# Performance work log

Measured on AMD Instinct MI355X. Metric: run time of the kernel, lower is better.

Reference implementation:

```python
import jax, jax.numpy as jnp
import numpy as np

B, T, C, H = 4, 2048, 1024, 16
D = C // H  # head dim = 64


def setup_inputs() -> dict:
    key = jax.random.key(0)
    k_x, k_wa, k_ba, k_wp, k_bp = jax.random.split(key, 5)
    s = 1.0 / np.sqrt(C)
    return {
        "x": jax.random.normal(k_x, (B, T, C), dtype=jnp.float32),
        "w_attn": jax.random.uniform(k_wa, (C, 3 * C), minval=-s, maxval=s, dtype=jnp.float32),
        "b_attn": jax.random.uniform(k_ba, (3 * C,), minval=-s, maxval=s, dtype=jnp.float32),
        "w_proj": jax.random.uniform(k_wp, (C, C), minval=-s, maxval=s, dtype=jnp.float32),
        "b_proj": jax.random.uniform(k_bp, (C,), minval=-s, maxval=s, dtype=jnp.float32),
    }


def reference(x, w_attn, b_attn, w_proj, b_proj):
    b, t, c = x.shape
    qkv = x @ w_attn + b_attn  # [b, t, 3c]
    q, k, v = jnp.split(qkv, 3, axis=-1)
    # [b, h, t, d]
    q = q.reshape(b, t, H, D).transpose(0, 2, 1, 3)
    k = k.reshape(b, t, H, D).transpose(0, 2, 1, 3)
    v = v.reshape(b, t, H, D).transpose(0, 2, 1, 3)
    scale = 1.0 / np.sqrt(D)
    logits = jnp.einsum("bhqd,bhkd->bhqk", q, k) * scale
    causal = jnp.tril(jnp.ones((t, t), dtype=bool))
    logits = jnp.where(causal, logits, jnp.finfo(logits.dtype).min)
    attn = jax.nn.softmax(logits, axis=-1)
    y = jnp.einsum("bhqk,bhkd->bhqd", attn, v)
    y = y.transpose(0, 2, 1, 3).reshape(b, t, c)
    return y @ w_proj + b_proj
```

## Files before the change

kernel.cpp:

```cpp
#include <hip/hip_runtime.h>


using u16 = unsigned short;
using u32 = unsigned int;
using bf16x8 = __attribute__((ext_vector_type(8))) __bf16;
using f32x4  = __attribute__((ext_vector_type(4))) float;
using f32x16 = __attribute__((ext_vector_type(16))) float;
using u16x8  = __attribute__((ext_vector_type(8))) u16;
using u16x4  = __attribute__((ext_vector_type(4))) u16;
using u32x2  = __attribute__((ext_vector_type(2))) u32;
using u32x4  = __attribute__((ext_vector_type(4))) u32;
using fvec4  = __attribute__((ext_vector_type(4))) float;

__device__ __forceinline__ u16 f2bf(float f) {
  u32 u = __builtin_bit_cast(u32, f);
  u32 r = (u + 0x7FFFu + ((u >> 16) & 1u)) >> 16;
  return (u16)r;
}

__device__ __forceinline__ u32 cvtpk(float lo, float hi) {
  u32 r;
  asm("v_cvt_pk_bf16_f32 %0, %1, %2" : "=v"(r) : "v"(lo), "v"(hi));
  return r;
}

__device__ __forceinline__ f32x4 mfma16(bf16x8 a, bf16x8 b, f32x4 c) {
  return __builtin_amdgcn_mfma_f32_16x16x32_bf16(a, b, c, 0, 0, 0);
}

__device__ __forceinline__ f32x16 mfma32(bf16x8 a, bf16x8 b, f32x16 c) {
  return __builtin_amdgcn_mfma_f32_32x32x16_bf16(a, b, c, 0, 0, 0);
}

__device__ __forceinline__ void gld16(const u16* g, u16* l) {
  __builtin_amdgcn_global_load_lds(
      (const __attribute__((address_space(1))) void*)g,
      (__attribute__((address_space(3))) void*)l, 16, 0, 0);
}

__device__ __forceinline__ void lgkm_barrier() {
  asm volatile("s_waitcnt lgkmcnt(0)" ::: "memory");
  __builtin_amdgcn_s_barrier();
  __builtin_amdgcn_sched_barrier(0);
}

__global__ __launch_bounds__(256) void conv_kernel(
    const float* __restrict__ in, u16* __restrict__ out) {
  const size_t i = ((size_t)blockIdx.x * 256 + threadIdx.x) * 8;
  fvec4 a = *(const fvec4*)(in + i);
  fvec4 b = *(const fvec4*)(in + i + 4);
  u16x8 h;
#pragma unroll
  for (int j = 0; j < 4; ++j) { h[j] = f2bf(a[j]); h[4 + j] = f2bf(b[j]); }
  *(u16x8*)(out + i) = h;
}

__global__ __launch_bounds__(256) void transpose_conv_kernel(
    const float* __restrict__ W, u16* __restrict__ Wt, int K, int N) {
  __shared__ float tile[32][33];
  const int n0 = blockIdx.x * 32, k0 = blockIdx.y * 32;
  const int tx = threadIdx.x, ty = threadIdx.y;
#pragma unroll
  for (int j = 0; j < 4; ++j)
    tile[ty + j * 8][tx] = W[(size_t)(k0 + ty + j * 8) * N + n0 + tx];
  __syncthreads();
#pragma unroll
  for (int j = 0; j < 4; ++j)
    Wt[(size_t)(n0 + ty + j * 8) * K + k0 + tx] = f2bf(tile[tx][ty + j * 8]);
}

template <int NB, bool QKV>
__global__ __launch_bounds__(512, 2) void gemm256_kernel(
    const u16* __restrict__ A, const u16* __restrict__ Bt,
    const float* __restrict__ bias, void* __restrict__ Cp,
    u16* __restrict__ vt, int M, int N, int K) {
  constexpr float SC = 0.18033688011112042f;
  __shared__ u16 As[2][2][8192];
  __shared__ u16 Bs[2][2][NB * 2048];
  const int tid = threadIdx.x;
  const int l = tid & 63, w = tid >> 6;
  const int l15 = l & 15, l16 = l >> 4;
  const int wr = w >> 2, wc = w & 3;

  const u32 nwg = gridDim.x * gridDim.y;
  u32 f = blockIdx.y * gridDim.x + blockIdx.x;
  f = (f & 7) * (nwg >> 3) + (f >> 3);
  const int ntile = gridDim.x;
  const long mbase = (long)(f / ntile) * 256;
  const long nbase = (long)(f % ntile) * (NB * 64);

  const int raS0 = w * 16 + (l >> 2);
  const int raS1 = raS0 + 128;
  const int scS0 = ((l & 3) ^ ((raS0 >> 1) & 3)) * 8;
  const int scS1 = ((l & 3) ^ ((raS1 >> 1) & 3)) * 8;
  const u16* gA0 = A + (mbase + raS0) * (long)K + scS0;
  const u16* gA1 = A + (mbase + raS1) * (long)K + scS1;
  const u16* gB0 = Bt + (nbase + raS0) * (long)K + scS0;
  const u16* gB1 = Bt + (nbase + raS1) * (long)K + scS1;

  const int raA = wr * 128 + l15;
  const int offA = raA * 32 + ((l16 ^ ((raA >> 1) & 3)) * 8);
  const int raB = wc * (NB * 16) + l15;
  const int offB = raB * 32 + ((l16 ^ ((raB >> 1) & 3)) * 8);

  f32x4 acc[8][NB] = {};
  bf16x8 af[4], bq[NB];
  const int NT = K >> 6;

#define STAGE_A(sb, ks, koff)                       \
  gld16(gA0 + (koff), &As[sb][ks][tid * 8]);        \
  gld16(gA1 + (koff), &As[sb][ks][tid * 8 + 4096]);

#define STAGE_B(sb, ks, koff)                                          \
  gld16(gB0 + (koff), &Bs[sb][ks][tid * 8]);                           \
  if constexpr (NB == 4) gld16(gB1 + (koff), &Bs[sb][ks][tid * 8 + 4096]);

#define DSA(cb, mh, ks)                                              \
  { _Pragma("unroll") for (int i_ = 0; i_ < 4; ++i_)                 \
      af[i_] = *(const bf16x8*)&As[cb][ks][offA + ((mh)*4 + i_) * 512]; }

#define DSB(cb, ks)                                                  \
  { _Pragma("unroll") for (int j_ = 0; j_ < NB; ++j_)                \
      bq[j_] = *(const bf16x8*)&Bs[cb][ks][offB + j_ * 512]; }

#define CLUSTER(mh)                                                            \
  __builtin_amdgcn_s_setprio(1);                                               \
  _Pragma("unroll") for (int i_ = 0; i_ < 4; ++i_)                             \
    _Pragma("unroll") for (int j_ = 0; j_ < NB; ++j_)                          \
      acc[(mh)*4 + i_][j_] = mfma16(af[i_], bq[j_], acc[(mh)*4 + i_][j_]);     \
  __builtin_amdgcn_s_setprio(0);

#define WAITVM()                                                         \
  if constexpr (NB == 4) { asm volatile("s_waitcnt vmcnt(4)" ::: "memory"); } \
  else { asm volatile("s_waitcnt vmcnt(3)" ::: "memory"); }

#define BAR_LGKM()                                        \
  __builtin_amdgcn_sched_barrier(0);                      \
  __builtin_amdgcn_s_barrier();                           \
  asm volatile("s_waitcnt lgkmcnt(0)" ::: "memory");      \
  __builtin_amdgcn_sched_barrier(0)

#define BAR_END()                     \
  __builtin_amdgcn_sched_barrier(0);  \
  __builtin_amdgcn_s_barrier()

  STAGE_A(0, 0, 0);
  STAGE_B(0, 0, 0);
  STAGE_A(0, 1, 32);
  STAGE_B(0, 1, 32);
  WAITVM();
  __builtin_amdgcn_s_barrier();

  for (int t = 0; t < NT - 1; ++t) {
    const int cb = t & 1, sb = cb ^ 1;
    const long kn = (long)(t + 1) * 64;
    DSA(cb, 0, 0); DSB(cb, 0);
    STAGE_A(sb, 0, kn);
    BAR_LGKM();
    CLUSTER(0);
    BAR_END();
    DSA(cb, 1, 0);
    STAGE_B(sb, 0, kn);
    BAR_LGKM();
    CLUSTER(1);
    WAITVM();
    BAR_END();
    DSA(cb, 0, 1); DSB(cb, 1);
    STAGE_A(sb, 1, kn + 32);
    BAR_LGKM();
    CLUSTER(0);
    BAR_END();
    DSA(cb, 1, 1);
    STAGE_B(sb, 1, kn + 32);
    BAR_LGKM();
    CLUSTER(1);
    WAITVM();
    BAR_END();
  }
  {
    const int cb = (NT - 1) & 1;
    DSA(cb, 0, 0); DSB(cb, 0);
    BAR_LGKM();
    CLUSTER(0);
    BAR_END();
    DSA(cb, 1, 0);
    BAR_LGKM();
    CLUSTER(1);
    asm volatile("s_waitcnt vmcnt(0)" ::: "memory");
    BAR_END();
    DSA(cb, 0, 1); DSB(cb, 1);
    BAR_LGKM();
    CLUSTER(0);
    BAR_END();
    DSA(cb, 1, 1);
    BAR_LGKM();
    CLUSTER(1);
  }
#undef STAGE_A
#undef STAGE_B
#undef DSA
#undef DSB
#undef CLUSTER
#undef WAITVM
#undef BAR_LGKM
#undef BAR_END

  if constexpr (QKV) {
    const bool isv = (nbase >= 2048);
#pragma unroll
    for (int mi = 0; mi < 8; ++mi) {
#pragma unroll
      for (int ni = 0; ni < NB; ++ni) {
        const long m0 = mbase + wr * 128 + mi * 16 + l16 * 4;
        const int n = (int)nbase + wc * (NB * 16) + ni * 16 + l15;
        const float bv = bias[n];
        if (!isv) {
          u16* qkp = (u16*)Cp;
          const float sc = (n < 1024) ? SC : 1.0f;
#pragma unroll
          for (int r = 0; r < 4; ++r)
            qkp[(m0 + r) * 2048 + n] = f2bf((acc[mi][ni][r] + bv) * sc);
        } else {
          const int vc = n - 2048, hh = vc >> 6, dd = vc & 63;
          const int bb = (int)(m0 >> 11), t0 = (int)(m0 & 2047);
          u16x4 pk;
#pragma unroll
          for (int r = 0; r < 4; ++r) pk[r] = f2bf(acc[mi][ni][r] + bv);
          *(u16x4*)(vt + ((size_t)(bb * 16 + hh) * 64 + dd) * 2048 + t0) = pk;
        }
      }
    }
  } else {
#pragma unroll
    for (int mi = 0; mi < 8; ++mi) {
#pragma unroll
      for (int ni = 0; ni < NB; ++ni) {
        const long row0 = mbase + wr * 128 + mi * 16 + l16 * 4;
        const long col = nbase + wc * (NB * 16) + ni * 16 + l15;
        const float bv = bias[col];
#pragma unroll
        for (int r = 0; r < 4; ++r)
          ((float*)Cp)[(row0 + r) * (long)N + col] = acc[mi][ni][r] + bv;
      }
    }
  }
}

__global__ __launch_bounds__(256, 2) void flash_kernel(
    const u16* __restrict__ qk, const u16* __restrict__ vt, u16* __restrict__ attn_out) {
  constexpr float MFIX = 4.0f;
  __shared__ u16 Ks[2][64 * 64];
  __shared__ u16 Vs[2][64 * 64];
  const int tid = threadIdx.x;
  const int lane = tid & 63, w = tid >> 6;
  const int l31 = lane & 31, hi = lane >> 5;
  const int xorv = (l31 & 7) << 4;

  const u32 i = blockIdx.y * 8 + blockIdx.x;
  const int jj = i >> 3;
  const int bh = (i & 7) | ((jj & 7) << 3);
  const int pair = (int)(i >> 6);
  const int b = bh >> 4, h = bh & 15;
  const u16* qbase = qk + (size_t)b * 2048 * 2048 + h * 64;
  const u16* kbase = qbase + 1024;
  const u16* vbase = vt + (size_t)bh * 64 * 2048;
  u16* obase = attn_out + (size_t)b * 2048 * 1024 + h * 64;

  const int r0 = tid >> 3, c0 = (tid & 7) * 8;
  const int sco = ((c0 * 2) ^ ((r0 & 7) << 4)) >> 1;

  int cur = 0;
  for (int half = 0; half < 2; ++half) {
    const int qt = half ? (15 - pair) : pair;
    const int nt = 2 * qt + 2;
    const int qr0 = qt * 128 + w * 32;
    const int q = qr0 + l31;

    bf16x8 qf[4];
#pragma unroll
    for (int ds = 0; ds < 4; ++ds)
      qf[ds] = *(const bf16x8*)(qbase + (size_t)q * 2048 + ds * 16 + hi * 8);

    f32x16 oacc[2] = {};
    float lsum = 0.f;

    u16x8 kreg[2], vreg[2];
    kreg[0] = *(const u16x8*)(kbase + (size_t)r0 * 2048 + c0);
    kreg[1] = *(const u16x8*)(kbase + (size_t)(r0 + 32) * 2048 + c0);
    vreg[0] = *(const u16x8*)(vbase + (size_t)r0 * 2048 + c0);
    vreg[1] = *(const u16x8*)(vbase + (size_t)(r0 + 32) * 2048 + c0);

    for (int kt = 0; kt < nt; ++kt) {
      const int kb = kt * 64;
      *(u16x8*)(&Ks[cur][r0 * 64 + sco]) = kreg[0];
      *(u16x8*)(&Ks[cur][(r0 + 32) * 64 + sco]) = kreg[1];
      *(u16x8*)(&Vs[cur][r0 * 64 + sco]) = vreg[0];
      *(u16x8*)(&Vs[cur][(r0 + 32) * 64 + sco]) = vreg[1];
      lgkm_barrier();
      if (kt + 1 < nt) {
        const int nb = kb + 64;
        kreg[0] = *(const u16x8*)(kbase + (size_t)(nb + r0) * 2048 + c0);
        kreg[1] = *(const u16x8*)(kbase + (size_t)(nb + r0 + 32) * 2048 + c0);
        vreg[0] = *(const u16x8*)(vbase + (size_t)r0 * 2048 + nb + c0);
        vreg[1] = *(const u16x8*)(vbase + (size_t)(r0 + 32) * 2048 + nb + c0);
      }

      f32x16 s0 = {}, s1 = {};
      __builtin_amdgcn_s_setprio(1);
#pragma unroll
      for (int ds = 0; ds < 4; ++ds) {
        const int col = (ds * 32 + hi * 16) ^ xorv;
        bf16x8 k0 = *(const bf16x8*)((const char*)&Ks[cur][0] + l31 * 128 + col);
        bf16x8 k1 = *(const bf16x8*)((const char*)&Ks[cur][0] + (32 + l31) * 128 + col);
        s0 = mfma32(k0, qf[ds], s0);
        s1 = mfma32(k1, qf[ds], s1);
      }
      __builtin_amdgcn_s_setprio(0);

      if (kb + 63 > qr0) {
#pragma unroll
        for (int r = 0; r < 16; ++r) {
          const int crow = (r & 3) + 8 * (r >> 2) + 4 * hi;
          if (kb + crow > q) s0[r] = -1e30f;
          if (kb + 32 + crow > q) s1[r] = -1e30f;
        }
      }

      float p0[16], p1[16];
      float ps = 0.f;
#pragma unroll
      for (int r = 0; r < 16; ++r) {
        p0[r] = exp2f(s0[r] - MFIX);
        p1[r] = exp2f(s1[r] - MFIX);
        ps += p0[r] + p1[r];
      }
      lsum += ps;

      bf16x8 pf[4];
#pragma unroll
      for (int kh = 0; kh < 2; ++kh) {
#pragma unroll
        for (int c = 0; c < 2; ++c) {
          const float* pp = kh ? p1 : p0;
          const int bs = c * 8;
          u32 L0 = cvtpk(pp[bs + 0], pp[bs + 1]);
          u32 L1 = cvtpk(pp[bs + 2], pp[bs + 3]);
          u32 L2 = cvtpk(pp[bs + 4], pp[bs + 5]);
          u32 L3 = cvtpk(pp[bs + 6], pp[bs + 7]);
          asm("v_permlane32_swap_b32 %0, %1" : "+v"(L0), "+v"(L2));
          asm("v_permlane32_swap_b32 %0, %1" : "+v"(L1), "+v"(L3));
          u32x4 pk = {L0, L1, L2, L3};
          pf[kh * 2 + c] = __builtin_bit_cast(bf16x8, pk);
        }
      }

      __builtin_amdgcn_s_setprio(1);
#pragma unroll
      for (int dh = 0; dh < 2; ++dh) {
#pragma unroll
        for (int ks = 0; ks < 4; ++ks) {
          const int col = (ks * 32 + hi * 16) ^ xorv;
          bf16x8 vf = *(const bf16x8*)((const char*)&Vs[cur][0] + (dh * 32 + l31) * 128 + col);
          oacc[dh] = mfma32(vf, pf[ks], oacc[dh]);
        }
      }
      __builtin_amdgcn_s_setprio(0);
      cur ^= 1;
    }

    lsum += __shfl_xor(lsum, 32);
    const float inv = 1.0f / lsum;
    u16* orow = obase + (size_t)q * 1024;
#pragma unroll
    for (int dh = 0; dh < 2; ++dh) {
#pragma unroll
      for (int jq = 0; jq < 4; ++jq) {
        u32x2 pk;
        pk[0] = cvtpk(oacc[dh][jq * 4 + 0] * inv, oacc[dh][jq * 4 + 1] * inv);
        pk[1] = cvtpk(oacc[dh][jq * 4 + 2] * inv, oacc[dh][jq * 4 + 3] * inv);
        *(u32x2*)(orow + dh * 32 + 8 * jq + 4 * hi) = pk;
      }
    }
  }
}

extern "C" void kernel_launch(void* const* d_in, const int* in_sizes, int n_in,
                              void* d_out, int out_size, void* d_ws, size_t ws_size,
                              hipStream_t stream) {
  (void)in_sizes; (void)n_in; (void)out_size; (void)ws_size;
  const float* x      = (const float*)d_in[0];
  const float* w_attn = (const float*)d_in[1];
  const float* b_attn = (const float*)d_in[2];
  const float* w_proj = (const float*)d_in[3];
  const float* b_proj = (const float*)d_in[4];
  float* out = (float*)d_out;

  char* ws = (char*)d_ws;
  u16* qkbuf = (u16*)(ws);
  u16* vtbuf = (u16*)(ws + 33554432);
  u16* xbf   = (u16*)(ws + 50331648);
  u16* attnb = (u16*)(ws + 50331648);
  u16* wtA   = (u16*)(ws + 67108864);
  u16* wtP   = (u16*)(ws + 73400320);

  conv_kernel<<<4096, 256, 0, stream>>>(x, xbf);
  transpose_conv_kernel<<<dim3(3072 / 32, 1024 / 32), dim3(32, 8), 0, stream>>>(w_attn, wtA, 1024, 3072);
  transpose_conv_kernel<<<dim3(1024 / 32, 1024 / 32), dim3(32, 8), 0, stream>>>(w_proj, wtP, 1024, 1024);

  gemm256_kernel<4, true><<<dim3(3072 / 256, 8192 / 256), 512, 0, stream>>>(
      xbf, wtA, b_attn, qkbuf, vtbuf, 8192, 3072, 1024);

  flash_kernel<<<dim3(8, 64), 256, 0, stream>>>(qkbuf, vtbuf, attnb);

  gemm256_kernel<2, false><<<dim3(1024 / 128, 8192 / 256), 512, 0, stream>>>(
      attnb, wtP, b_proj, out, nullptr, 8192, 1024, 1024);
}
```

Before: 189.0 us.

## Replace 256-tile 8-wave GEMM with simpler 128x128 4-wave double-buffered GEMM

Swaps the hand-scheduled 256xN GEMM (512 threads, interleaved half-cluster LDS loads and barriers, K-step 64) for a plain 128x128 tile kernel with 256 threads, K-step 32 and a single double-buffered stage per iteration. It also changes the grids for both the QKV and output projection GEMMs. The simpler kernel cuts per-block LDS and register use and gives more blocks. The cost is lower data reuse per tile, more global traffic and less overlap, because each iteration now waits for the full prefetch before its barrier.

```diff
diff --git a/kernel.cpp b/kernel.cpp
--- a/kernel.cpp
+++ b/kernel.cpp
@@ -69,178 +69,111 @@
     Wt[(size_t)(n0 + ty + j * 8) * K + k0 + tx] = f2bf(tile[tx][ty + j * 8]);
 }
 
-template <int NB, bool QKV>
-__global__ __launch_bounds__(512, 2) void gemm256_kernel(
+template <bool QKV>
+__global__ __launch_bounds__(256) void gemm_kernel(
     const u16* __restrict__ A, const u16* __restrict__ Bt,
     const float* __restrict__ bias, void* __restrict__ Cp,
     u16* __restrict__ vt, int M, int N, int K) {
   constexpr float SC = 0.18033688011112042f;
-  __shared__ u16 As[2][2][8192];
-  __shared__ u16 Bs[2][2][NB * 2048];
+  __shared__ u16 As[2][4096];
+  __shared__ u16 Bs[2][4096];
   const int tid = threadIdx.x;
   const int l = tid & 63, w = tid >> 6;
   const int l15 = l & 15, l16 = l >> 4;
-  const int wr = w >> 2, wc = w & 3;
+  const int wm = (w >> 1) * 64, wn = (w & 1) * 64;
 
   const u32 nwg = gridDim.x * gridDim.y;
   u32 f = blockIdx.y * gridDim.x + blockIdx.x;
   f = (f & 7) * (nwg >> 3) + (f >> 3);
-  const int ntile = gridDim.x;
-  const long mbase = (long)(f / ntile) * 256;
-  const long nbase = (long)(f % ntile) * (NB * 64);
-
-  const int raS0 = w * 16 + (l >> 2);
-  const int raS1 = raS0 + 128;
-  const int scS0 = ((l & 3) ^ ((raS0 >> 1) & 3)) * 8;
-  const int scS1 = ((l & 3) ^ ((raS1 >> 1) & 3)) * 8;
-  const u16* gA0 = A + (mbase + raS0) * (long)K + scS0;
-  const u16* gA1 = A + (mbase + raS1) * (long)K + scS1;
-  const u16* gB0 = Bt + (nbase + raS0) * (long)K + scS0;
-  const u16* gB1 = Bt + (nbase + raS1) * (long)K + scS1;
-
-  const int raA = wr * 128 + l15;
-  const int offA = raA * 32 + ((l16 ^ ((raA >> 1) & 3)) * 8);
-  const int raB = wc * (NB * 16) + l15;
-  const int offB = raB * 32 + ((l16 ^ ((raB >> 1) & 3)) * 8);
-
-  f32x4 acc[8][NB] = {};
-  bf16x8 af[4], bq[NB];
-  const int NT = K >> 6;
-
-#define STAGE_A(sb, ks, koff)                       \
-  gld16(gA0 + (koff), &As[sb][ks][tid * 8]);        \
-  gld16(gA1 + (koff), &As[sb][ks][tid * 8 + 4096]);
-
-#define STAGE_B(sb, ks, koff)                                          \
-  gld16(gB0 + (koff), &Bs[sb][ks][tid * 8]);                           \
-  if constexpr (NB == 4) gld16(gB1 + (koff), &Bs[sb][ks][tid * 8 + 4096]);
-
-#define DSA(cb, mh, ks)                                              \
-  { _Pragma("unroll") for (int i_ = 0; i_ < 4; ++i_)                 \
-      af[i_] = *(const bf16x8*)&As[cb][ks][offA + ((mh)*4 + i_) * 512]; }
-
-#define DSB(cb, ks)                                                  \
-  { _Pragma("unroll") for (int j_ = 0; j_ < NB; ++j_)                \
-      bq[j_] = *(const bf16x8*)&Bs[cb][ks][offB + j_ * 512]; }
-
-#define CLUSTER(mh)                                                            \
-  __builtin_amdgcn_s_setprio(1);                                               \
-  _Pragma("unroll") for (int i_ = 0; i_ < 4; ++i_)                             \
-    _Pragma("unroll") for (int j_ = 0; j_ < NB; ++j_)                          \
-      acc[(mh)*4 + i_][j_] = mfma16(af[i_], bq[j_], acc[(mh)*4 + i_][j_]);     \
-  __builtin_amdgcn_s_setprio(0);
-
-#define WAITVM()                                                         \
-  if constexpr (NB == 4) { asm volatile("s_waitcnt vmcnt(4)" ::: "memory"); } \
-  else { asm volatile("s_waitcnt vmcnt(3)" ::: "memory"); }
-
-#define BAR_LGKM()                                        \
-  __builtin_amdgcn_sched_barrier(0);                      \
-  __builtin_amdgcn_s_barrier();                           \
-  asm volatile("s_waitcnt lgkmcnt(0)" ::: "memory");      \
-  __builtin_amdgcn_sched_barrier(0)
-
-#define BAR_END()                     \
-  __builtin_amdgcn_sched_barrier(0);  \
-  __builtin_amdgcn_s_barrier()
-
-  STAGE_A(0, 0, 0);
-  STAGE_B(0, 0, 0);
-  STAGE_A(0, 1, 32);
-  STAGE_B(0, 1, 32);
-  WAITVM();
+  const long mbase = (long)(f / gridDim.x) * 128;
+  const long nbase = (long)(f % gridDim.x) * 128;
+
+  const int srow = tid >> 2;
+  const int scol = ((tid & 3) ^ ((srow >> 1) & 3)) * 8;
+  const u16* gA0 = A + (mbase + srow) * (long)K + scol;
+  const u16* gA1 = gA0 + 64 * (long)K;
+  const u16* gB0 = Bt + (nbase + srow) * (long)K + scol;
+  const u16* gB1 = gB0 + 64 * (long)K;
+
+  f32x4 acc[4][4] = {};
+  const int NT = K >> 5;
+
+#define STAGE(buf, koff)                         \
+  gld16(gA0 + (koff), &As[buf][tid * 8]);        \
+  gld16(gA1 + (koff), &As[buf][tid * 8 + 2048]); \
+  gld16(gB0 + (koff), &Bs[buf][tid * 8]);        \
+  gld16(gB1 + (koff), &Bs[buf][tid * 8 + 2048]);
+
+  STAGE(0, 0);
+  asm volatile("s_waitcnt vmcnt(0)" ::: "memory");
   __builtin_amdgcn_s_barrier();
 
-  for (int t = 0; t < NT - 1; ++t) {
-    const int cb = t & 1, sb = cb ^ 1;
-    const long kn = (long)(t + 1) * 64;
-    DSA(cb, 0, 0); DSB(cb, 0);
-    STAGE_A(sb, 0, kn);
-    BAR_LGKM();
-    CLUSTER(0);
-    BAR_END();
-    DSA(cb, 1, 0);
-    STAGE_B(sb, 0, kn);
-    BAR_LGKM();
-    CLUSTER(1);
-    WAITVM();
-    BAR_END();
-    DSA(cb, 0, 1); DSB(cb, 1);
-    STAGE_A(sb, 1, kn + 32);
-    BAR_LGKM();
-    CLUSTER(0);
-    BAR_END();
-    DSA(cb, 1, 1);
-    STAGE_B(sb, 1, kn + 32);
-    BAR_LGKM();
-    CLUSTER(1);
-    WAITVM();
-    BAR_END();
+  for (int t = 0; t < NT; ++t) {
+    const int cur = t & 1;
+    if (t + 1 < NT) { STAGE(cur ^ 1, (t + 1) * 32); }
+
+    bf16x8 af[4], bfr[4];
+#pragma unroll
+    for (int i = 0; i < 4; ++i) {
+      const int row = wm + i * 16 + l15;
+      af[i] = *(const bf16x8*)(&As[cur][row * 32 + ((l16 ^ ((row >> 1) & 3)) * 8)]);
+    }
+#pragma unroll
+    for (int j = 0; j < 4; ++j) {
+      const int row = wn + j * 16 + l15;
+      bfr[j] = *(const bf16x8*)(&Bs[cur][row * 32 + ((l16 ^ ((row >> 1) & 3)) * 8)]);
+    }
+    asm volatile("s_waitcnt lgkmcnt(0)" ::: "memory");
+    __builtin_amdgcn_sched_barrier(0);
+    __builtin_amdgcn_s_setprio(1);
+#pragma unroll
+    for (int i = 0; i < 4; ++i)
+#pragma unroll
+      for (int j = 0; j < 4; ++j)
+        acc[i][j] = mfma16(af[i], bfr[j], acc[i][j]);
+    __builtin_amdgcn_s_setprio(0);
+    __builtin_amdgcn_sched_barrier(0);
+    if (t + 1 < NT) { asm volatile("s_waitcnt vmcnt(0)" ::: "memory"); }
+    __builtin_amdgcn_s_barrier();
   }
-  {
-    const int cb = (NT - 1) & 1;
-    DSA(cb, 0, 0); DSB(cb, 0);
-    BAR_LGKM();
-    CLUSTER(0);
-    BAR_END();
-    DSA(cb, 1, 0);
-    BAR_LGKM();
-    CLUSTER(1);
-    asm volatile("s_waitcnt vmcnt(0)" ::: "memory");
-    BAR_END();
-    DSA(cb, 0, 1); DSB(cb, 1);
-    BAR_LGKM();
-    CLUSTER(0);
-    BAR_END();
-    DSA(cb, 1, 1);
-    BAR_LGKM();
-    CLUSTER(1);
-  }
-#undef STAGE_A
-#undef STAGE_B
-#undef DSA
-#undef DSB
-#undef CLUSTER
-#undef WAITVM
-#undef BAR_LGKM
-#undef BAR_END
+#undef STAGE
 
   if constexpr (QKV) {
     const bool isv = (nbase >= 2048);
 #pragma unroll
-    for (int mi = 0; mi < 8; ++mi) {
-#pragma unroll
-      for (int ni = 0; ni < NB; ++ni) {
-        const long m0 = mbase + wr * 128 + mi * 16 + l16 * 4;
-        const int n = (int)nbase + wc * (NB * 16) + ni * 16 + l15;
+    for (int i = 0; i < 4; ++i) {
+#pragma unroll
+      for (int j = 0; j < 4; ++j) {
+        const long m0 = mbase + wm + i * 16 + l16 * 4;
+        const int n = (int)nbase + wn + j * 16 + l15;
         const float bv = bias[n];
         if (!isv) {
           u16* qkp = (u16*)Cp;
           const float sc = (n < 1024) ? SC : 1.0f;
 #pragma unroll
           for (int r = 0; r < 4; ++r)
-            qkp[(m0 + r) * 2048 + n] = f2bf((acc[mi][ni][r] + bv) * sc);
+            qkp[(m0 + r) * 2048 + n] = f2bf((acc[i][j][r] + bv) * sc);
         } else {
           const int vc = n - 2048, hh = vc >> 6, dd = vc & 63;
           const int bb = (int)(m0 >> 11), t0 = (int)(m0 & 2047);
           u16x4 pk;
 #pragma unroll
-          for (int r = 0; r < 4; ++r) pk[r] = f2bf(acc[mi][ni][r] + bv);
+          for (int r = 0; r < 4; ++r) pk[r] = f2bf(acc[i][j][r] + bv);
           *(u16x4*)(vt + ((size_t)(bb * 16 + hh) * 64 + dd) * 2048 + t0) = pk;
         }
       }
     }
   } else {
 #pragma unroll
-    for (int mi = 0; mi < 8; ++mi) {
-#pragma unroll
-      for (int ni = 0; ni < NB; ++ni) {
-        const long row0 = mbase + wr * 128 + mi * 16 + l16 * 4;
-        const long col = nbase + wc * (NB * 16) + ni * 16 + l15;
+    for (int i = 0; i < 4; ++i) {
+#pragma unroll
+      for (int j = 0; j < 4; ++j) {
+        const long row0 = mbase + wm + i * 16 + l16 * 4;
+        const long col = nbase + wn + j * 16 + l15;
         const float bv = bias[col];
 #pragma unroll
         for (int r = 0; r < 4; ++r)
-          ((float*)Cp)[(row0 + r) * (long)N + col] = acc[mi][ni][r] + bv;
+          ((float*)Cp)[(row0 + r) * (long)N + col] = acc[i][j][r] + bv;
       }
     }
   }
@@ -407,11 +340,11 @@
   transpose_conv_kernel<<<dim3(3072 / 32, 1024 / 32), dim3(32, 8), 0, stream>>>(w_attn, wtA, 1024, 3072);
   transpose_conv_kernel<<<dim3(1024 / 32, 1024 / 32), dim3(32, 8), 0, stream>>>(w_proj, wtP, 1024, 1024);
 
-  gemm256_kernel<4, true><<<dim3(3072 / 256, 8192 / 256), 512, 0, stream>>>(
+  gemm_kernel<true><<<dim3(3072 / 128, 8192 / 128), 256, 0, stream>>>(
       xbf, wtA, b_attn, qkbuf, vtbuf, 8192, 3072, 1024);
 
   flash_kernel<<<dim3(8, 64), 256, 0, stream>>>(qkbuf, vtbuf, attnb);
 
-  gemm256_kernel<2, false><<<dim3(1024 / 128, 8192 / 256), 512, 0, stream>>>(
+  gemm_kernel<false><<<dim3(1024 / 128, 8192 / 128), 256, 0, stream>>>(
       attnb, wtP, b_proj, out, nullptr, 8192, 1024, 1024);
 }
```

After: 177.9 us. -5.8%, faster.
